# Kernel tuning notes

Measured on AMD Instinct MI355X. Metric: run time of the kernel, lower is better.

## Reference

```python
import jax, jax.numpy as jnp
import numpy as np

B_, L_, D_, N_ = 2, 2048, 512, 64

def setup_inputs() -> dict:
    key = jax.random.key(0)
    ks = jax.random.split(key, 6)
    s = 1.0 / np.sqrt(D_)
    return {
        "x": jax.random.normal(ks[0], (B_, L_, D_), dtype=jnp.float32),
        "W1": jax.random.normal(ks[1], (D_, D_), dtype=jnp.float32) * s,
        "b1": jnp.zeros((D_,), dtype=jnp.float32),
        "W2": jax.random.normal(ks[2], (D_, N_), dtype=jnp.float32) * s,
        "b2": jnp.zeros((N_,), dtype=jnp.float32),
        "W3": jax.random.normal(ks[3], (D_, N_), dtype=jnp.float32) * s,
        "b3": jnp.zeros((N_,), dtype=jnp.float32),
        "A": jax.random.normal(ks[4], (D_, N_), dtype=jnp.float32) * (1.0 / np.sqrt(N_)),
    }

def reference(x, W1, b1, W2, b2, W3, b3, A):
    # Projections (faithful to fc2/fc3/fc1 in the torch module)
    B = x @ W2 + b2                                  # (b, l, n)
    C = x @ W3 + b3                                  # (b, l, n)
    delta = jax.nn.softplus(x @ W1 + b1)             # (b, l, d)
    # Discretization
    dB = jnp.einsum('bld,bln->bldn', delta, B)       # (b, l, d, n)
    dA = jnp.exp(jnp.einsum('bld,dn->bldn', delta, A))  # (b, l, d, n)
    # h is initialized to zeros in the original forward, so the dA*h term
    # contributes exactly zero; kept for faithfulness to the source math.
    h = dA * 0.0 + x[..., None] * dB                 # (b, l, d, n)
    y = jnp.einsum('bln,bldn->bld', C, h)            # (b, l, d)
    return y
```

## Files before the change

kernel.cpp:

```cpp
#include <hip/hip_runtime.h>
#include <math.h>

#define DDIM 512

typedef _Float16 f16;
typedef _Float16 f16x4 __attribute__((ext_vector_type(4)));
typedef _Float16 f16x8 __attribute__((ext_vector_type(8)));
typedef float f32x4 __attribute__((ext_vector_type(4)));

__device__ __forceinline__ float softplusf(float v) {
    return (v > 20.0f) ? v : log1pf(__expf(v));
}

__global__ __launch_bounds__(256) void prep_w(
    const float* __restrict__ W1, const float* __restrict__ W2,
    const float* __restrict__ W3, f16* __restrict__ w1t, f16* __restrict__ w23)
{
    __shared__ __align__(16) f16 lt[32][520];
    const int tid  = threadIdx.x;
    const int wb   = blockIdx.x;
    const int wv   = tid >> 6;
    const int lane = tid & 63;
    const int q    = lane >> 4;
    const int l15  = lane & 15;

    const float* src; int srcRS, col0; f16* dst;
    if (wb < 16)      { src = W1; srcRS = DDIM; col0 = wb * 32;
                        dst = w1t + (size_t)wb * 2 * 16 * 512; }
    else if (wb < 18) { src = W2; srcRS = 64;  col0 = (wb - 16) * 32;
                        dst = w23 + (size_t)(wb - 16) * 2 * 16 * 512; }
    else              { src = W3; srcRS = 64;  col0 = (wb - 18) * 32;
                        dst = w23 + (size_t)(4 + (wb - 18) * 2) * 16 * 512; }
#pragma unroll
    for (int i = 0; i < 16; ++i) {
        int f  = tid + 256 * i;
        int k  = f >> 3;
        int c4 = (f & 7) * 4;
        float4 v = *(const float4*)(src + (size_t)k * srcRS + col0 + c4);
        lt[c4 + 0][k] = (f16)v.x; lt[c4 + 1][k] = (f16)v.y;
        lt[c4 + 2][k] = (f16)v.z; lt[c4 + 3][k] = (f16)v.w;
    }
    __syncthreads();
#pragma unroll
    for (int j = 0; j < 8; ++j) {
        int s   = wv * 8 + j;
        int ntL = s >> 4;
        int kt  = s & 15;
        f16x8 vv = *(const f16x8*)&lt[ntL * 16 + l15][kt * 32 + q * 8];
        *(f16x8*)(dst + (size_t)(ntL * 16 + kt) * 512 + lane * 8) = vv;
    }
}

__global__ __launch_bounds__(256) void s_kernel(
    const float* __restrict__ x, const f16* __restrict__ w23,
    const float* __restrict__ b2, const float* __restrict__ b3,
    f16* __restrict__ xh, float* __restrict__ s_out)
{
    __shared__ __align__(16) f16 xs[16][520];
    __shared__ float sred[64];

    const int tid  = threadIdx.x;
    const int wv   = tid >> 6;
    const int lane = tid & 63;
    const int q    = lane >> 4;
    const int l15  = lane & 15;
    const int mtG  = blockIdx.x;
    const int tb   = mtG * 16;

    {
        const int row = tid >> 4, cg = tid & 15;
        const float* xr = x + (size_t)(tb + row) * DDIM;
#pragma unroll
        for (int i = 0; i < 8; ++i) {
            int col = cg * 4 + i * 64;
            float4 v = *(const float4*)(xr + col);
            f16x4 h = {(f16)v.x, (f16)v.y, (f16)v.z, (f16)v.w};
            *(f16x4*)&xs[row][col] = h;
        }
    }
    __syncthreads();

#pragma unroll
    for (int j = 0; j < 4; ++j) {
        int kt = wv * 4 + j;
        f16x8 vv = *(const f16x8*)&xs[l15][kt * 32 + q * 8];
        *(f16x8*)(xh + (size_t)(mtG * 16 + kt) * 512 + lane * 8) = vv;
    }

    f32x4 acc0 = (f32x4){0.f, 0.f, 0.f, 0.f};
    f32x4 acc1 = (f32x4){0.f, 0.f, 0.f, 0.f};
    const f16* wB = w23 + (size_t)(wv    ) * 16 * 512 + lane * 8;
    const f16* wC = w23 + (size_t)(wv + 4) * 16 * 512 + lane * 8;
#pragma unroll
    for (int kt = 0; kt < 16; ++kt) {
        f16x8 a  = *(const f16x8*)&xs[l15][kt * 32 + q * 8];
        f16x8 bB = *(const f16x8*)(wB + (size_t)kt * 512);
        f16x8 bC = *(const f16x8*)(wC + (size_t)kt * 512);
        acc0 = __builtin_amdgcn_mfma_f32_16x16x32_f16(a, bB, acc0, 0, 0, 0);
        acc1 = __builtin_amdgcn_mfma_f32_16x16x32_f16(a, bC, acc1, 0, 0, 0);
    }

    float b2v = b2[wv * 16 + l15];
    float b3v = b3[wv * 16 + l15];
#pragma unroll
    for (int r = 0; r < 4; ++r) {
        float p = (acc0[r] + b2v) * (acc1[r] + b3v);
        p += __shfl_xor(p, 1); p += __shfl_xor(p, 2);
        p += __shfl_xor(p, 4); p += __shfl_xor(p, 8);
        if (l15 == 0) sred[wv * 16 + q * 4 + r] = p;
    }
    __syncthreads();
    if (tid < 16)
        s_out[tb + tid] = sred[tid] + sred[16 + tid] + sred[32 + tid] + sred[48 + tid];
}

__global__ __launch_bounds__(512) void y_kernel(
    const f16* __restrict__ xh, const f16* __restrict__ w1t,
    const float* __restrict__ x, const float* __restrict__ b1,
    const float* __restrict__ s_in, float* __restrict__ y)
{
    const int tid  = threadIdx.x;
    const int wv   = tid >> 6;
    const int lane = tid & 63;
    const int q    = lane >> 4;
    const int l15  = lane & 15;
    const int mt   = wv & 3;
    const int nh   = wv >> 2;
    const int cB   = blockIdx.x;
    const int rB   = blockIdx.y;

    const f16* aP  = xh  + (size_t)((rB * 4 + mt) * 16) * 512 + lane * 8;
    const f16* bP0 = w1t + (size_t)((cB * 4 + nh * 2 + 0) * 16) * 512 + lane * 8;
    const f16* bP1 = w1t + (size_t)((cB * 4 + nh * 2 + 1) * 16) * 512 + lane * 8;

    f32x4 acc0 = (f32x4){0.f, 0.f, 0.f, 0.f};
    f32x4 acc1 = (f32x4){0.f, 0.f, 0.f, 0.f};
#pragma unroll
    for (int kt = 0; kt < 16; ++kt) {
        f16x8 a  = *(const f16x8*)(aP  + (size_t)kt * 512);
        f16x8 b0 = *(const f16x8*)(bP0 + (size_t)kt * 512);
        f16x8 b1v = *(const f16x8*)(bP1 + (size_t)kt * 512);
        acc0 = __builtin_amdgcn_mfma_f32_16x16x32_f16(a, b0,  acc0, 0, 0, 0);
        acc1 = __builtin_amdgcn_mfma_f32_16x16x32_f16(a, b1v, acc1, 0, 0, 0);
    }

    const int d0 = cB * 64 + (nh * 2 + 0) * 16 + l15;
    const int d1 = cB * 64 + (nh * 2 + 1) * 16 + l15;
    const float bb0 = b1[d0], bb1 = b1[d1];
#pragma unroll
    for (int r = 0; r < 4; ++r) {
        int token = rB * 64 + mt * 16 + q * 4 + r;
        float st = s_in[token];
        const float* xr = x + (size_t)token * DDIM;
        float*       yr = y + (size_t)token * DDIM;
        yr[d0] = xr[d0] * softplusf(acc0[r] + bb0) * st;
        yr[d1] = xr[d1] * softplusf(acc1[r] + bb1) * st;
    }
}

extern "C" void kernel_launch(void* const* d_in, const int* in_sizes, int n_in,
                              void* d_out, int out_size, void* d_ws, size_t ws_size,
                              hipStream_t stream)
{
    (void)n_in; (void)out_size; (void)ws_size;
    const float* x  = (const float*)d_in[0];
    const float* W1 = (const float*)d_in[1];
    const float* b1 = (const float*)d_in[2];
    const float* W2 = (const float*)d_in[3];
    const float* b2 = (const float*)d_in[4];
    const float* W3 = (const float*)d_in[5];
    const float* b3 = (const float*)d_in[6];
    float* y = (float*)d_out;

    char* ws  = (char*)d_ws;
    f16* xh   = (f16*)(ws);
    f16* w1t  = (f16*)(ws + (4 << 20));
    f16* w23  = (f16*)(ws + (4 << 20) + (512 << 10));
    float* sv = (float*)(ws + (5 << 20));

    const int M = in_sizes[0] / DDIM;

    prep_w<<<20, 256, 0, stream>>>(W1, W2, W3, w1t, w23);
    s_kernel<<<M / 16, 256, 0, stream>>>(x, w23, b2, b3, xh, sv);
    y_kernel<<<dim3(8, M / 64), 512, 0, stream>>>(xh, w1t, x, b1, sv, y);
}
```

Baseline: 94.74 us.

## Fuse weight prep, s-reduction and y GEMM into one cooperative kernel

Replaces the three separate launches (weight transpose/convert, x conversion plus B·C dot product, and the W1 GEMM with softplus epilogue) with a single cooperative kernel of 512 blocks that uses grid-wide syncs between phases. The x-to-fp16 conversion and weight transposition now run concurrently in phase one, which removes two kernel launch gaps and the serialisation of prep before s. It adds two grid barriers and cooperative-launch overhead, and it hardcodes the grid size to M=4096 tokens instead of deriving it from the input size.

```diff
diff --git a/kernel.cpp b/kernel.cpp
--- a/kernel.cpp
+++ b/kernel.cpp
@@ -1,5 +1,8 @@
 #include <hip/hip_runtime.h>
+#include <hip/hip_cooperative_groups.h>
 #include <math.h>
+
+namespace cg = cooperative_groups;
 
 #define DDIM 512
 
@@ -12,149 +15,145 @@
     return (v > 20.0f) ? v : log1pf(__expf(v));
 }
 
-__global__ __launch_bounds__(256) void prep_w(
-    const float* __restrict__ W1, const float* __restrict__ W2,
-    const float* __restrict__ W3, f16* __restrict__ w1t, f16* __restrict__ w23)
+__global__ __launch_bounds__(512, 4) void fused_kernel(
+    const float* __restrict__ x,  const float* __restrict__ W1,
+    const float* __restrict__ b1, const float* __restrict__ W2,
+    const float* __restrict__ b2, const float* __restrict__ W3,
+    const float* __restrict__ b3,
+    f16* __restrict__ xh, f16* __restrict__ w1t, f16* __restrict__ w23,
+    float* __restrict__ sv, float* __restrict__ y)
 {
-    __shared__ __align__(16) f16 lt[32][520];
+    __shared__ __align__(16) char smem[33536];
+    f16 (*xs)[520]  = (f16(*)[520])smem;
+    f16 (*lt)[520]  = (f16(*)[520])smem;
+    float* sred     = (float*)(smem + 33280);
+
     const int tid  = threadIdx.x;
-    const int wb   = blockIdx.x;
+    const int bid  = blockIdx.x;
     const int wv   = tid >> 6;
     const int lane = tid & 63;
     const int q    = lane >> 4;
     const int l15  = lane & 15;
 
-    const float* src; int srcRS, col0; f16* dst;
-    if (wb < 16)      { src = W1; srcRS = DDIM; col0 = wb * 32;
-                        dst = w1t + (size_t)wb * 2 * 16 * 512; }
-    else if (wb < 18) { src = W2; srcRS = 64;  col0 = (wb - 16) * 32;
-                        dst = w23 + (size_t)(wb - 16) * 2 * 16 * 512; }
-    else              { src = W3; srcRS = 64;  col0 = (wb - 18) * 32;
-                        dst = w23 + (size_t)(4 + (wb - 18) * 2) * 16 * 512; }
-#pragma unroll
-    for (int i = 0; i < 16; ++i) {
-        int f  = tid + 256 * i;
-        int k  = f >> 3;
-        int c4 = (f & 7) * 4;
-        float4 v = *(const float4*)(src + (size_t)k * srcRS + col0 + c4);
-        lt[c4 + 0][k] = (f16)v.x; lt[c4 + 1][k] = (f16)v.y;
-        lt[c4 + 2][k] = (f16)v.z; lt[c4 + 3][k] = (f16)v.w;
-    }
-    __syncthreads();
-#pragma unroll
-    for (int j = 0; j < 8; ++j) {
-        int s   = wv * 8 + j;
-        int ntL = s >> 4;
-        int kt  = s & 15;
-        f16x8 vv = *(const f16x8*)&lt[ntL * 16 + l15][kt * 32 + q * 8];
-        *(f16x8*)(dst + (size_t)(ntL * 16 + kt) * 512 + lane * 8) = vv;
-    }
-}
+    cg::grid_group grid = cg::this_grid();
 
-__global__ __launch_bounds__(256) void s_kernel(
-    const float* __restrict__ x, const f16* __restrict__ w23,
-    const float* __restrict__ b2, const float* __restrict__ b3,
-    f16* __restrict__ xh, float* __restrict__ s_out)
-{
-    __shared__ __align__(16) f16 xs[16][520];
-    __shared__ float sred[64];
-
-    const int tid  = threadIdx.x;
-    const int wv   = tid >> 6;
-    const int lane = tid & 63;
-    const int q    = lane >> 4;
-    const int l15  = lane & 15;
-    const int mtG  = blockIdx.x;
-    const int tb   = mtG * 16;
-
-    {
-        const int row = tid >> 4, cg = tid & 15;
+    if (bid < 256) {
+        const int tb  = bid * 16;
+        const int row = tid >> 5;
+        const int cg4 = (tid & 31) * 4;
         const float* xr = x + (size_t)(tb + row) * DDIM;
 #pragma unroll
-        for (int i = 0; i < 8; ++i) {
-            int col = cg * 4 + i * 64;
+        for (int i = 0; i < 4; ++i) {
+            int col = cg4 + i * 128;
             float4 v = *(const float4*)(xr + col);
             f16x4 h = {(f16)v.x, (f16)v.y, (f16)v.z, (f16)v.w};
             *(f16x4*)&xs[row][col] = h;
         }
-    }
-    __syncthreads();
-
+        __syncthreads();
 #pragma unroll
-    for (int j = 0; j < 4; ++j) {
-        int kt = wv * 4 + j;
-        f16x8 vv = *(const f16x8*)&xs[l15][kt * 32 + q * 8];
-        *(f16x8*)(xh + (size_t)(mtG * 16 + kt) * 512 + lane * 8) = vv;
+        for (int j = 0; j < 2; ++j) {
+            int kt = wv * 2 + j;
+            f16x8 vv = *(const f16x8*)&xs[l15][kt * 32 + q * 8];
+            *(f16x8*)(xh + (size_t)(bid * 16 + kt) * 512 + lane * 8) = vv;
+        }
+    } else if (bid < 276) {
+        const int wb = bid - 256;
+        const float* src; int srcRS, col0; f16* dst;
+        if (wb < 16)      { src = W1; srcRS = DDIM; col0 = wb * 32;
+                            dst = w1t + (size_t)wb * 2 * 16 * 512; }
+        else if (wb < 18) { src = W2; srcRS = 64;  col0 = (wb - 16) * 32;
+                            dst = w23 + (size_t)(wb - 16) * 2 * 16 * 512; }
+        else              { src = W3; srcRS = 64;  col0 = (wb - 18) * 32;
+                            dst = w23 + (size_t)(4 + (wb - 18) * 2) * 16 * 512; }
+#pragma unroll
+        for (int i = 0; i < 8; ++i) {
+            int f  = tid + 512 * i;
+            int k  = f >> 3;
+            int c4 = (f & 7) * 4;
+            float4 v = *(const float4*)(src + (size_t)k * srcRS + col0 + c4);
+            lt[c4 + 0][k] = (f16)v.x; lt[c4 + 1][k] = (f16)v.y;
+            lt[c4 + 2][k] = (f16)v.z; lt[c4 + 3][k] = (f16)v.w;
+        }
+        __syncthreads();
+#pragma unroll
+        for (int j = 0; j < 4; ++j) {
+            int s   = wv * 4 + j;
+            int ntL = s >> 4;
+            int kt  = s & 15;
+            f16x8 vv = *(const f16x8*)&lt[ntL * 16 + l15][kt * 32 + q * 8];
+            *(f16x8*)(dst + (size_t)(ntL * 16 + kt) * 512 + lane * 8) = vv;
+        }
     }
 
-    f32x4 acc0 = (f32x4){0.f, 0.f, 0.f, 0.f};
-    f32x4 acc1 = (f32x4){0.f, 0.f, 0.f, 0.f};
-    const f16* wB = w23 + (size_t)(wv    ) * 16 * 512 + lane * 8;
-    const f16* wC = w23 + (size_t)(wv + 4) * 16 * 512 + lane * 8;
+    __threadfence();
+    grid.sync();
+
+    if (bid < 256) {
+        const int tb = bid * 16;
+        if (wv < 4) {
+            f32x4 acc0 = (f32x4){0.f, 0.f, 0.f, 0.f};
+            f32x4 acc1 = (f32x4){0.f, 0.f, 0.f, 0.f};
+            const f16* wB = w23 + (size_t)(wv    ) * 16 * 512 + lane * 8;
+            const f16* wC = w23 + (size_t)(wv + 4) * 16 * 512 + lane * 8;
 #pragma unroll
-    for (int kt = 0; kt < 16; ++kt) {
-        f16x8 a  = *(const f16x8*)&xs[l15][kt * 32 + q * 8];
-        f16x8 bB = *(const f16x8*)(wB + (size_t)kt * 512);
-        f16x8 bC = *(const f16x8*)(wC + (size_t)kt * 512);
-        acc0 = __builtin_amdgcn_mfma_f32_16x16x32_f16(a, bB, acc0, 0, 0, 0);
-        acc1 = __builtin_amdgcn_mfma_f32_16x16x32_f16(a, bC, acc1, 0, 0, 0);
+            for (int kt = 0; kt < 16; ++kt) {
+                f16x8 a  = *(const f16x8*)&xs[l15][kt * 32 + q * 8];
+                f16x8 bB = *(const f16x8*)(wB + (size_t)kt * 512);
+                f16x8 bC = *(const f16x8*)(wC + (size_t)kt * 512);
+                acc0 = __builtin_amdgcn_mfma_f32_16x16x32_f16(a, bB, acc0, 0, 0, 0);
+                acc1 = __builtin_amdgcn_mfma_f32_16x16x32_f16(a, bC, acc1, 0, 0, 0);
+            }
+            float b2v = b2[wv * 16 + l15];
+            float b3v = b3[wv * 16 + l15];
+#pragma unroll
+            for (int r = 0; r < 4; ++r) {
+                float p = (acc0[r] + b2v) * (acc1[r] + b3v);
+                p += __shfl_xor(p, 1); p += __shfl_xor(p, 2);
+                p += __shfl_xor(p, 4); p += __shfl_xor(p, 8);
+                if (l15 == 0) sred[wv * 16 + q * 4 + r] = p;
+            }
+        }
+        __syncthreads();
+        if (tid < 16)
+            sv[tb + tid] = sred[tid] + sred[16 + tid] + sred[32 + tid] + sred[48 + tid];
     }
 
-    float b2v = b2[wv * 16 + l15];
-    float b3v = b3[wv * 16 + l15];
+    __threadfence();
+    grid.sync();
+
+    {
+        const int cB = bid & 7;
+        const int rB = bid >> 3;
+        const int mt = wv & 3;
+        const int nh = wv >> 2;
+
+        const f16* aP  = xh  + (size_t)((rB * 4 + mt) * 16) * 512 + lane * 8;
+        const f16* bP0 = w1t + (size_t)((cB * 4 + nh * 2 + 0) * 16) * 512 + lane * 8;
+        const f16* bP1 = w1t + (size_t)((cB * 4 + nh * 2 + 1) * 16) * 512 + lane * 8;
+
+        f32x4 acc0 = (f32x4){0.f, 0.f, 0.f, 0.f};
+        f32x4 acc1 = (f32x4){0.f, 0.f, 0.f, 0.f};
 #pragma unroll
-    for (int r = 0; r < 4; ++r) {
-        float p = (acc0[r] + b2v) * (acc1[r] + b3v);
-        p += __shfl_xor(p, 1); p += __shfl_xor(p, 2);
-        p += __shfl_xor(p, 4); p += __shfl_xor(p, 8);
-        if (l15 == 0) sred[wv * 16 + q * 4 + r] = p;
-    }
-    __syncthreads();
-    if (tid < 16)
-        s_out[tb + tid] = sred[tid] + sred[16 + tid] + sred[32 + tid] + sred[48 + tid];
-}
+        for (int kt = 0; kt < 16; ++kt) {
+            f16x8 a  = *(const f16x8*)(aP  + (size_t)kt * 512);
+            f16x8 b0 = *(const f16x8*)(bP0 + (size_t)kt * 512);
+            f16x8 bb = *(const f16x8*)(bP1 + (size_t)kt * 512);
+            acc0 = __builtin_amdgcn_mfma_f32_16x16x32_f16(a, b0, acc0, 0, 0, 0);
+            acc1 = __builtin_amdgcn_mfma_f32_16x16x32_f16(a, bb, acc1, 0, 0, 0);
+        }
 
-__global__ __launch_bounds__(512) void y_kernel(
-    const f16* __restrict__ xh, const f16* __restrict__ w1t,
-    const float* __restrict__ x, const float* __restrict__ b1,
-    const float* __restrict__ s_in, float* __restrict__ y)
-{
-    const int tid  = threadIdx.x;
-    const int wv   = tid >> 6;
-    const int lane = tid & 63;
-    const int q    = lane >> 4;
-    const int l15  = lane & 15;
-    const int mt   = wv & 3;
-    const int nh   = wv >> 2;
-    const int cB   = blockIdx.x;
-    const int rB   = blockIdx.y;
-
-    const f16* aP  = xh  + (size_t)((rB * 4 + mt) * 16) * 512 + lane * 8;
-    const f16* bP0 = w1t + (size_t)((cB * 4 + nh * 2 + 0) * 16) * 512 + lane * 8;
-    const f16* bP1 = w1t + (size_t)((cB * 4 + nh * 2 + 1) * 16) * 512 + lane * 8;
-
-    f32x4 acc0 = (f32x4){0.f, 0.f, 0.f, 0.f};
-    f32x4 acc1 = (f32x4){0.f, 0.f, 0.f, 0.f};
+        const int d0 = cB * 64 + (nh * 2 + 0) * 16 + l15;
+        const int d1 = cB * 64 + (nh * 2 + 1) * 16 + l15;
+        const float bb0 = b1[d0], bb1 = b1[d1];
 #pragma unroll
-    for (int kt = 0; kt < 16; ++kt) {
-        f16x8 a  = *(const f16x8*)(aP  + (size_t)kt * 512);
-        f16x8 b0 = *(const f16x8*)(bP0 + (size_t)kt * 512);
-        f16x8 b1v = *(const f16x8*)(bP1 + (size_t)kt * 512);
-        acc0 = __builtin_amdgcn_mfma_f32_16x16x32_f16(a, b0,  acc0, 0, 0, 0);
-        acc1 = __builtin_amdgcn_mfma_f32_16x16x32_f16(a, b1v, acc1, 0, 0, 0);
-    }
-
-    const int d0 = cB * 64 + (nh * 2 + 0) * 16 + l15;
-    const int d1 = cB * 64 + (nh * 2 + 1) * 16 + l15;
-    const float bb0 = b1[d0], bb1 = b1[d1];
-#pragma unroll
-    for (int r = 0; r < 4; ++r) {
-        int token = rB * 64 + mt * 16 + q * 4 + r;
-        float st = s_in[token];
-        const float* xr = x + (size_t)token * DDIM;
-        float*       yr = y + (size_t)token * DDIM;
-        yr[d0] = xr[d0] * softplusf(acc0[r] + bb0) * st;
-        yr[d1] = xr[d1] * softplusf(acc1[r] + bb1) * st;
+        for (int r = 0; r < 4; ++r) {
+            int token = rB * 64 + mt * 16 + q * 4 + r;
+            float st = sv[token];
+            const float* xr = x + (size_t)token * DDIM;
+            float*       yr = y + (size_t)token * DDIM;
+            yr[d0] = xr[d0] * softplusf(acc0[r] + bb0) * st;
+            yr[d1] = xr[d1] * softplusf(acc1[r] + bb1) * st;
+        }
     }
 }
 
@@ -162,7 +161,7 @@
                               void* d_out, int out_size, void* d_ws, size_t ws_size,
                               hipStream_t stream)
 {
-    (void)n_in; (void)out_size; (void)ws_size;
+    (void)n_in; (void)out_size; (void)ws_size; (void)in_sizes;
     const float* x  = (const float*)d_in[0];
     const float* W1 = (const float*)d_in[1];
     const float* b1 = (const float*)d_in[2];
@@ -178,9 +177,9 @@
     f16* w23  = (f16*)(ws + (4 << 20) + (512 << 10));
     float* sv = (float*)(ws + (5 << 20));
 
-    const int M = in_sizes[0] / DDIM;
-
-    prep_w<<<20, 256, 0, stream>>>(W1, W2, W3, w1t, w23);
-    s_kernel<<<M / 16, 256, 0, stream>>>(x, w23, b2, b3, xh, sv);
-    y_kernel<<<dim3(8, M / 64), 512, 0, stream>>>(xh, w1t, x, b1, sv, y);
+    void* args[] = { (void*)&x, (void*)&W1, (void*)&b1, (void*)&W2, (void*)&b2,
+                     (void*)&W3, (void*)&b3, (void*)&xh, (void*)&w1t, (void*)&w23,
+                     (void*)&sv, (void*)&y };
+    hipLaunchCooperativeKernel((const void*)fused_kernel,
+                               dim3(512), dim3(512), args, 0, stream);
 }
```

Result: slower. 370.2 us (+290.8%).

## Merge weight prep and s-projection into one kernel, read W2/W3 directly

Applied to the files above, without the earlier changes.

Folds the W1 transpose/convert work and the s computation into a single launch, with blocks 0-255 computing s and xh and blocks 256-271 preparing W1. The s blocks now load W2/W3 from fp32 global memory with strided scalar loads and convert them in registers, instead of using a pre-transposed f16 buffer. This removes one kernel launch and a dependency, at the cost of uncoalesced redundant weight reads in every s block. The grid size of 256 s-blocks is hardcoded rather than derived from M.

```diff
diff --git a/kernel.cpp b/kernel.cpp
--- a/kernel.cpp
+++ b/kernel.cpp
@@ -12,31 +12,87 @@
     return (v > 20.0f) ? v : log1pf(__expf(v));
 }
 
-__global__ __launch_bounds__(256) void prep_w(
-    const float* __restrict__ W1, const float* __restrict__ W2,
-    const float* __restrict__ W3, f16* __restrict__ w1t, f16* __restrict__ w23)
+__global__ __launch_bounds__(256) void k1_s_and_prep(
+    const float* __restrict__ x,  const float* __restrict__ W1,
+    const float* __restrict__ W2, const float* __restrict__ b2,
+    const float* __restrict__ W3, const float* __restrict__ b3,
+    f16* __restrict__ xh, f16* __restrict__ w1t, float* __restrict__ s_out)
 {
-    __shared__ __align__(16) f16 lt[32][520];
+    __shared__ __align__(16) char smem[34048];
+    f16 (*xs)[520] = (f16(*)[520])smem;
+    f16 (*lt)[520] = (f16(*)[520])smem;
+    float* sred    = (float*)(smem + 33536);
+
     const int tid  = threadIdx.x;
-    const int wb   = blockIdx.x;
+    const int bid  = blockIdx.x;
     const int wv   = tid >> 6;
     const int lane = tid & 63;
     const int q    = lane >> 4;
     const int l15  = lane & 15;
 
-    const float* src; int srcRS, col0; f16* dst;
-    if (wb < 16)      { src = W1; srcRS = DDIM; col0 = wb * 32;
-                        dst = w1t + (size_t)wb * 2 * 16 * 512; }
-    else if (wb < 18) { src = W2; srcRS = 64;  col0 = (wb - 16) * 32;
-                        dst = w23 + (size_t)(wb - 16) * 2 * 16 * 512; }
-    else              { src = W3; srcRS = 64;  col0 = (wb - 18) * 32;
-                        dst = w23 + (size_t)(4 + (wb - 18) * 2) * 16 * 512; }
+    if (bid < 256) {
+        const int tb  = bid * 16;
+        const int row = tid >> 4;
+        const int cg  = tid & 15;
+        const float* xr = x + (size_t)(tb + row) * DDIM;
+#pragma unroll
+        for (int i = 0; i < 8; ++i) {
+            int col = cg * 4 + i * 64;
+            float4 v = *(const float4*)(xr + col);
+            f16x4 h = {(f16)v.x, (f16)v.y, (f16)v.z, (f16)v.w};
+            *(f16x4*)&xs[row][col] = h;
+        }
+        __syncthreads();
+
+#pragma unroll
+        for (int j = 0; j < 4; ++j) {
+            int kt = wv * 4 + j;
+            f16x8 vv = *(const f16x8*)&xs[l15][kt * 32 + q * 8];
+            *(f16x8*)(xh + (size_t)(bid * 16 + kt) * 512 + lane * 8) = vv;
+        }
+
+        const int ncol = wv * 16 + l15;
+        f32x4 acc0 = (f32x4){0.f, 0.f, 0.f, 0.f};
+        f32x4 acc1 = (f32x4){0.f, 0.f, 0.f, 0.f};
+#pragma unroll
+        for (int kt = 0; kt < 16; ++kt) {
+            f16x8 a = *(const f16x8*)&xs[l15][kt * 32 + q * 8];
+            const float* p2 = W2 + (size_t)(kt * 32 + q * 8) * 64 + ncol;
+            const float* p3 = W3 + (size_t)(kt * 32 + q * 8) * 64 + ncol;
+            f16x8 bB, bC;
+#pragma unroll
+            for (int j = 0; j < 8; ++j) {
+                bB[j] = (f16)p2[j * 64];
+                bC[j] = (f16)p3[j * 64];
+            }
+            acc0 = __builtin_amdgcn_mfma_f32_16x16x32_f16(a, bB, acc0, 0, 0, 0);
+            acc1 = __builtin_amdgcn_mfma_f32_16x16x32_f16(a, bC, acc1, 0, 0, 0);
+        }
+        float b2v = b2[ncol];
+        float b3v = b3[ncol];
+#pragma unroll
+        for (int r = 0; r < 4; ++r) {
+            float p = (acc0[r] + b2v) * (acc1[r] + b3v);
+            p += __shfl_xor(p, 1); p += __shfl_xor(p, 2);
+            p += __shfl_xor(p, 4); p += __shfl_xor(p, 8);
+            if (l15 == 0) sred[wv * 16 + q * 4 + r] = p;
+        }
+        __syncthreads();
+        if (tid < 16)
+            s_out[tb + tid] = sred[tid] + sred[16 + tid] + sred[32 + tid] + sred[48 + tid];
+        return;
+    }
+
+    const int wb = bid - 256;
+    const float* src = W1;
+    const int col0 = wb * 32;
+    f16* dst = w1t + (size_t)wb * 2 * 16 * 512;
 #pragma unroll
     for (int i = 0; i < 16; ++i) {
         int f  = tid + 256 * i;
         int k  = f >> 3;
         int c4 = (f & 7) * 4;
-        float4 v = *(const float4*)(src + (size_t)k * srcRS + col0 + c4);
+        float4 v = *(const float4*)(src + (size_t)k * DDIM + col0 + c4);
         lt[c4 + 0][k] = (f16)v.x; lt[c4 + 1][k] = (f16)v.y;
         lt[c4 + 2][k] = (f16)v.z; lt[c4 + 3][k] = (f16)v.w;
     }
@@ -51,70 +107,7 @@
     }
 }
 
-__global__ __launch_bounds__(256) void s_kernel(
-    const float* __restrict__ x, const f16* __restrict__ w23,
-    const float* __restrict__ b2, const float* __restrict__ b3,
-    f16* __restrict__ xh, float* __restrict__ s_out)
-{
-    __shared__ __align__(16) f16 xs[16][520];
-    __shared__ float sred[64];
-
-    const int tid  = threadIdx.x;
-    const int wv   = tid >> 6;
-    const int lane = tid & 63;
-    const int q    = lane >> 4;
-    const int l15  = lane & 15;
-    const int mtG  = blockIdx.x;
-    const int tb   = mtG * 16;
-
-    {
-        const int row = tid >> 4, cg = tid & 15;
-        const float* xr = x + (size_t)(tb + row) * DDIM;
-#pragma unroll
-        for (int i = 0; i < 8; ++i) {
-            int col = cg * 4 + i * 64;
-            float4 v = *(const float4*)(xr + col);
-            f16x4 h = {(f16)v.x, (f16)v.y, (f16)v.z, (f16)v.w};
-            *(f16x4*)&xs[row][col] = h;
-        }
-    }
-    __syncthreads();
-
-#pragma unroll
-    for (int j = 0; j < 4; ++j) {
-        int kt = wv * 4 + j;
-        f16x8 vv = *(const f16x8*)&xs[l15][kt * 32 + q * 8];
-        *(f16x8*)(xh + (size_t)(mtG * 16 + kt) * 512 + lane * 8) = vv;
-    }
-
-    f32x4 acc0 = (f32x4){0.f, 0.f, 0.f, 0.f};
-    f32x4 acc1 = (f32x4){0.f, 0.f, 0.f, 0.f};
-    const f16* wB = w23 + (size_t)(wv    ) * 16 * 512 + lane * 8;
-    const f16* wC = w23 + (size_t)(wv + 4) * 16 * 512 + lane * 8;
-#pragma unroll
-    for (int kt = 0; kt < 16; ++kt) {
-        f16x8 a  = *(const f16x8*)&xs[l15][kt * 32 + q * 8];
-        f16x8 bB = *(const f16x8*)(wB + (size_t)kt * 512);
-        f16x8 bC = *(const f16x8*)(wC + (size_t)kt * 512);
-        acc0 = __builtin_amdgcn_mfma_f32_16x16x32_f16(a, bB, acc0, 0, 0, 0);
-        acc1 = __builtin_amdgcn_mfma_f32_16x16x32_f16(a, bC, acc1, 0, 0, 0);
-    }
-
-    float b2v = b2[wv * 16 + l15];
-    float b3v = b3[wv * 16 + l15];
-#pragma unroll
-    for (int r = 0; r < 4; ++r) {
-        float p = (acc0[r] + b2v) * (acc1[r] + b3v);
-        p += __shfl_xor(p, 1); p += __shfl_xor(p, 2);
-        p += __shfl_xor(p, 4); p += __shfl_xor(p, 8);
-        if (l15 == 0) sred[wv * 16 + q * 4 + r] = p;
-    }
-    __syncthreads();
-    if (tid < 16)
-        s_out[tb + tid] = sred[tid] + sred[16 + tid] + sred[32 + tid] + sred[48 + tid];
-}
-
-__global__ __launch_bounds__(512) void y_kernel(
+__global__ __launch_bounds__(512) void k2_y(
     const f16* __restrict__ xh, const f16* __restrict__ w1t,
     const float* __restrict__ x, const float* __restrict__ b1,
     const float* __restrict__ s_in, float* __restrict__ y)
@@ -139,9 +132,9 @@
     for (int kt = 0; kt < 16; ++kt) {
         f16x8 a  = *(const f16x8*)(aP  + (size_t)kt * 512);
         f16x8 b0 = *(const f16x8*)(bP0 + (size_t)kt * 512);
-        f16x8 b1v = *(const f16x8*)(bP1 + (size_t)kt * 512);
-        acc0 = __builtin_amdgcn_mfma_f32_16x16x32_f16(a, b0,  acc0, 0, 0, 0);
-        acc1 = __builtin_amdgcn_mfma_f32_16x16x32_f16(a, b1v, acc1, 0, 0, 0);
+        f16x8 bb = *(const f16x8*)(bP1 + (size_t)kt * 512);
+        acc0 = __builtin_amdgcn_mfma_f32_16x16x32_f16(a, b0, acc0, 0, 0, 0);
+        acc1 = __builtin_amdgcn_mfma_f32_16x16x32_f16(a, bb, acc1, 0, 0, 0);
     }
 
     const int d0 = cB * 64 + (nh * 2 + 0) * 16 + l15;
@@ -175,12 +168,10 @@
     char* ws  = (char*)d_ws;
     f16* xh   = (f16*)(ws);
     f16* w1t  = (f16*)(ws + (4 << 20));
-    f16* w23  = (f16*)(ws + (4 << 20) + (512 << 10));
     float* sv = (float*)(ws + (5 << 20));
 
     const int M = in_sizes[0] / DDIM;
 
-    prep_w<<<20, 256, 0, stream>>>(W1, W2, W3, w1t, w23);
-    s_kernel<<<M / 16, 256, 0, stream>>>(x, w23, b2, b3, xh, sv);
-    y_kernel<<<dim3(8, M / 64), 512, 0, stream>>>(xh, w1t, x, b1, sv, y);
+    k1_s_and_prep<<<272, 256, 0, stream>>>(x, W1, W2, b2, W3, b3, xh, w1t, sv);
+    k2_y<<<dim3(8, M / 64), 512, 0, stream>>>(xh, w1t, x, b1, sv, y);
 }
```

After: 100.3 us. 1.06x slower.
